# Performance work log

Measured on AMD Instinct MI355X. Metric: run time of the kernel, lower is better.

## Reference

```python
import jax, jax.numpy as jnp
import numpy as np

N = 50000
D = 128           # feature_dim
H = 8             # num_heads
DH = D // H       # head_dim = 16
K = 32            # k_neighbors
FFN = int(D * 1.5)  # 192
TAU_NEG = 0.6
BETA = 1.5
LN_EPS = 1e-5


def layer_norm(x, g, b):
    mu = jnp.mean(x, axis=-1, keepdims=True)
    var = jnp.mean((x - mu) ** 2, axis=-1, keepdims=True)
    return (x - mu) * jax.lax.rsqrt(var + LN_EPS) * g + b


def setup_inputs() -> dict:
    key = jax.random.key(0)
    ks = jax.random.split(key, 12)
    s = 1.0 / np.sqrt(D)
    inp = {
        "features": jax.random.normal(ks[0], (N, D), dtype=jnp.float32),
        "knn_indices": jax.random.randint(ks[1], (N, K), 0, N, dtype=jnp.int64 if jax.config.jax_enable_x64 else jnp.int32),
        "spatial_distances": jax.random.uniform(ks[2], (N, K), dtype=jnp.float32) * 8.0,
        "Wq": jax.random.normal(ks[3], (D, D), dtype=jnp.float32) * s,
        "Wk": jax.random.normal(ks[4], (D, D), dtype=jnp.float32) * s,
        "Wv": jax.random.normal(ks[5], (D, D), dtype=jnp.float32) * s,
        "Wo": jax.random.normal(ks[6], (D, D), dtype=jnp.float32) * s,
        "bo": jnp.zeros((D,), dtype=jnp.float32),
        "ln1_g": jnp.ones((D,), dtype=jnp.float32),
        "ln1_b": jnp.zeros((D,), dtype=jnp.float32),
        "W1": jax.random.normal(ks[7], (D, FFN), dtype=jnp.float32) * s,
        "b1": jnp.zeros((FFN,), dtype=jnp.float32),
        "W2": jax.random.normal(ks[8], (FFN, D), dtype=jnp.float32) * (1.0 / np.sqrt(FFN)),
        "b2": jnp.zeros((D,), dtype=jnp.float32),
        "ln2_g": jnp.ones((D,), dtype=jnp.float32),
        "ln2_b": jnp.zeros((D,), dtype=jnp.float32),
    }
    return inp


def reference(features, knn_indices, spatial_distances, Wq, Wk, Wv, Wo, bo,
              ln1_g, ln1_b, W1, b1, W2, b2, ln2_g, ln2_b):
    n = features.shape[0]
    Q = (features @ Wq).reshape(n, H, DH)           # (N,H,dh)
    Kp = (features @ Wk).reshape(n, H, DH)
    Vp = (features @ Wv).reshape(n, H, DH)

    K_local = Kp[knn_indices]                        # (N,K,H,dh) irregular gather
    V_local = Vp[knn_indices]                        # (N,K,H,dh)

    raw_scores = jnp.einsum("nhd,nkhd->nhk", Q, K_local) / np.sqrt(DH)  # (N,H,K)

    # per-head spatial decay: 1 / 2^(h+1)
    head_scalings = (0.5 ** jnp.arange(1, H + 1, dtype=features.dtype))  # (H,)
    scaled_dist = spatial_distances[:, None, :] * head_scalings[None, :, None]  # (N,H,K)

    attn_pos = jax.nn.softmax(raw_scores - scaled_dist, axis=-1)
    attn_neg = jax.nn.softmax((-raw_scores - scaled_dist) / TAU_NEG, axis=-1)
    attn = attn_pos - BETA * attn_neg                # (N,H,K); dropout is identity in eval

    attended = jnp.einsum("nhk,nkhd->nhd", attn, V_local).reshape(n, D)

    x = attended @ Wo + bo + features
    x = layer_norm(x, ln1_g, ln1_b)

    h = jax.nn.gelu(x @ W1 + b1, approximate=False)
    ffn_out = h @ W2 + b2
    out = layer_norm(ffn_out + x, ln2_g, ln2_b)
    return out
```

## Files before the change

### kernel.cpp

```cpp
#include <hip/hip_runtime.h>
#include <hip/hip_fp16.h>
#include <cmath>

typedef __attribute__((ext_vector_type(8))) _Float16 f16x8;
typedef __attribute__((ext_vector_type(4))) float f32x4;
typedef __attribute__((ext_vector_type(4))) unsigned int u32x4;

__device__ __forceinline__ unsigned int pkh(float a, float b) {
    __half2 h = __floats2half2_rn(a, b);
    return *(unsigned int*)&h;
}
__device__ __forceinline__ float gelu_fast(float x) {
    float w = x * fmaf(x * x, 0.1029377202f, 2.302085565f);
    return x * __builtin_amdgcn_rcpf(1.0f + exp2f(-w));
}
__device__ __forceinline__ __half2 shfl8h(__half2 x, int m) {
    int xi = *(int*)&x;
    int yi = __shfl_xor(xi, m, 8);
    return *(__half2*)&yi;
}

__global__ __launch_bounds__(256, 1) void k_prep(
    const float* __restrict__ Wq, const float* __restrict__ Wk, const float* __restrict__ Wv,
    const float* __restrict__ Wo, const float* __restrict__ W1, const float* __restrict__ W2,
    unsigned short* __restrict__ wsz)
{
    int idx = blockIdx.x * 256 + threadIdx.x;
    if (idx >= 28672) return;
    int f = idx >> 1;
    const int half = idx & 1;
    const float* W; unsigned short* dst; int M, KS, fl;
    if (f < 2048)       { W = Wq; dst = wsz;         M = 128; KS = 4; fl = f; }
    else if (f < 4096)  { W = Wk; dst = wsz + 16384; M = 128; KS = 4; fl = f - 2048; }
    else if (f < 6144)  { W = Wv; dst = wsz + 32768; M = 128; KS = 4; fl = f - 4096; }
    else if (f < 8192)  { W = Wo; dst = wsz + 49152; M = 128; KS = 4; fl = f - 6144; }
    else if (f < 11264) { W = W1; dst = wsz + 65536; M = 192; KS = 4; fl = f - 8192; }
    else                { W = W2; dst = wsz + 90112; M = 128; KS = 6; fl = f - 11264; }
    const int l  = fl & 63;
    const int ks = (fl >> 6) % KS;
    const int ct = (fl >> 6) / KS;
    const int k0 = ks * 32 + (l >> 4) * 8 + half * 4;
    const int col = ct * 16 + (l & 15);
    unsigned short tmp[4];
    #pragma unroll
    for (int j = 0; j < 4; ++j) {
        __half hh = __float2half(W[(size_t)(k0 + j) * M + col]);
        tmp[j] = *(unsigned short*)&hh;
    }
    ((uint2*)dst)[fl * 2 + half] = *(uint2*)tmp;
}

__global__ __launch_bounds__(256, 8) void k_qkv(
    const float* __restrict__ feat, const unsigned short* __restrict__ wsz,
    unsigned short* __restrict__ Qb, unsigned short* __restrict__ KVb, int n)
{
    const int w = threadIdx.x >> 6, lane = threadIdx.x & 63;
    const int lrow = lane & 15, kgrp = lane >> 4;
    const int node = blockIdx.x * 64 + w * 16 + lrow;
    const bool valid = node < n;

    f16x8 bfr[4];
    #pragma unroll
    for (int ks = 0; ks < 4; ++ks) {
        float4 lo = make_float4(0.f, 0.f, 0.f, 0.f), hi = lo;
        if (valid) {
            const float* p = feat + (size_t)node * 128 + ks * 32 + kgrp * 8;
            lo = *(const float4*)p;
            hi = *(const float4*)(p + 4);
        }
        f16x8 b;
        b[0] = (_Float16)lo.x; b[1] = (_Float16)lo.y; b[2] = (_Float16)lo.z; b[3] = (_Float16)lo.w;
        b[4] = (_Float16)hi.x; b[5] = (_Float16)hi.y; b[6] = (_Float16)hi.z; b[7] = (_Float16)hi.w;
        bfr[ks] = b;
    }

    for (int mat = 0; mat < 3; ++mat) {
        const unsigned short* wb = wsz + mat * 16384;
        f32x4 acc[8];
        #pragma unroll
        for (int ct = 0; ct < 8; ++ct) acc[ct] = (f32x4){0.f, 0.f, 0.f, 0.f};
        #pragma unroll
        for (int ct = 0; ct < 8; ++ct)
            #pragma unroll
            for (int ks = 0; ks < 4; ++ks) {
                f16x8 afr = *(const f16x8*)(wb + ((size_t)(ct * 4 + ks) * 64 + lane) * 8);
                acc[ct] = __builtin_amdgcn_mfma_f32_16x16x32_f16(afr, bfr[ks], acc[ct], 0, 0, 0);
            }
        if (valid) {
            unsigned short* O = (mat == 0) ? (Qb + (size_t)node * 128)
                              : (KVb + (size_t)node * 256 + (mat == 2 ? 128 : 0));
            #pragma unroll
            for (int ct = 0; ct < 8; ++ct) {
                int col = ct * 16 + kgrp * 4;
                *((uint2*)(O + col)) =
                    make_uint2(pkh(acc[ct][0], acc[ct][1]), pkh(acc[ct][2], acc[ct][3]));
            }
        }
    }
}

__global__ __launch_bounds__(256, 4) void k_attn(
    const unsigned short* __restrict__ Qb, const unsigned short* __restrict__ KVb,
    const int* __restrict__ knn, const float* __restrict__ dist,
    unsigned short* __restrict__ attf, int n)
{
    const int lane = threadIdx.x & 63;
    const int node = blockIdx.x * 4 + (threadIdx.x >> 6);
    if (node >= n) return;
    const int h = lane >> 3, r = lane & 7;
    const float L2E = 1.4426950408889634f;
    const float hsl = exp2f(-(float)(h + 1)) * L2E;

    int idx[4]; float sdl[4];
    #pragma unroll
    for (int jj = 0; jj < 4; ++jj) {
        int j = r + jj * 8;
        idx[jj] = __builtin_nontemporal_load(knn + (size_t)node * 32 + j);
        sdl[jj] = __builtin_nontemporal_load(dist + (size_t)node * 32 + j) * hsl;
    }

    const unsigned short* qp = Qb + (size_t)node * 128 + h * 16;
    __half2 q2[8];
    *((u32x4*)&q2[0]) = __builtin_nontemporal_load((const u32x4*)qp);
    *((u32x4*)&q2[4]) = __builtin_nontemporal_load((const u32x4*)(qp + 8));

    uint4 k0[4], k1[4], v0[4], v1[4];
    #pragma unroll
    for (int jj = 0; jj < 4; ++jj) {
        const unsigned short* kvp = KVb + (size_t)idx[jj] * 256 + h * 16;
        k0[jj] = *(const uint4*)kvp;
        k1[jj] = *(const uint4*)(kvp + 8);
        v0[jj] = *(const uint4*)(kvp + 128);
        v1[jj] = *(const uint4*)(kvp + 136);
    }

    float ap[4], an[4];
    #pragma unroll
    for (int jj = 0; jj < 4; ++jj) {
        const __half2* ka = (const __half2*)&k0[jj];
        const __half2* kb = (const __half2*)&k1[jj];
        __half2 s0 = __hmul2(q2[0], ka[0]);
        s0 = __hfma2(q2[1], ka[1], s0);
        s0 = __hfma2(q2[2], ka[2], s0);
        s0 = __hfma2(q2[3], ka[3], s0);
        __half2 s1 = __hmul2(q2[4], kb[0]);
        s1 = __hfma2(q2[5], kb[1], s1);
        s1 = __hfma2(q2[6], kb[2], s1);
        s1 = __hfma2(q2[7], kb[3], s1);
        float s = __low2float(s0) + __high2float(s0) + __low2float(s1) + __high2float(s1);
        float rawl = s * (0.25f * L2E);
        ap[jj] = rawl - sdl[jj];
        an[jj] = (-rawl - sdl[jj]) * (1.0f / 0.6f);
    }

    float mp = fmaxf(fmaxf(ap[0], ap[1]), fmaxf(ap[2], ap[3]));
    float mn = fmaxf(fmaxf(an[0], an[1]), fmaxf(an[2], an[3]));
    #pragma unroll
    for (int msk = 1; msk < 8; msk <<= 1) {
        mp = fmaxf(mp, __shfl_xor(mp, msk, 8));
        mn = fmaxf(mn, __shfl_xor(mn, msk, 8));
    }
    float ep[4], en[4], sp = 0.f, sn = 0.f;
    #pragma unroll
    for (int jj = 0; jj < 4; ++jj) {
        ep[jj] = exp2f(ap[jj] - mp); sp += ep[jj];
        en[jj] = exp2f(an[jj] - mn); sn += en[jj];
    }
    #pragma unroll
    for (int msk = 1; msk < 8; msk <<= 1) {
        sp += __shfl_xor(sp, msk, 8);
        sn += __shfl_xor(sn, msk, 8);
    }
    const float isp = 1.0f / sp;
    const float isn = 1.5f / sn;

    __half2 acc2[8];
    #pragma unroll
    for (int i = 0; i < 8; ++i) acc2[i] = __float2half2_rn(0.f);
    #pragma unroll
    for (int jj = 0; jj < 4; ++jj) {
        float wgt = ep[jj] * isp - en[jj] * isn;
        __half2 w2 = __float2half2_rn(wgt);
        const __half2* va = (const __half2*)&v0[jj];
        const __half2* vb = (const __half2*)&v1[jj];
        acc2[0] = __hfma2(w2, va[0], acc2[0]);
        acc2[1] = __hfma2(w2, va[1], acc2[1]);
        acc2[2] = __hfma2(w2, va[2], acc2[2]);
        acc2[3] = __hfma2(w2, va[3], acc2[3]);
        acc2[4] = __hfma2(w2, vb[0], acc2[4]);
        acc2[5] = __hfma2(w2, vb[1], acc2[5]);
        acc2[6] = __hfma2(w2, vb[2], acc2[6]);
        acc2[7] = __hfma2(w2, vb[3], acc2[7]);
    }
    #pragma unroll
    for (int i = 0; i < 8; ++i) {
        acc2[i] = __hadd2(acc2[i], shfl8h(acc2[i], 1));
        acc2[i] = __hadd2(acc2[i], shfl8h(acc2[i], 2));
        acc2[i] = __hadd2(acc2[i], shfl8h(acc2[i], 4));
    }
    if (r == 0) {
        const int g = node >> 4, lrow = node & 15;
        unsigned short* op = attf + (size_t)g * 2048 + (h >> 1) * 512 + (h & 1) * 256 + lrow * 8;
        __builtin_nontemporal_store(*(u32x4*)&acc2[0], (u32x4*)op);
        __builtin_nontemporal_store(*(u32x4*)&acc2[4], (u32x4*)(op + 128));
    }
}

__global__ __launch_bounds__(256, 4) void k_tail(
    const unsigned short* __restrict__ attf, const float* __restrict__ feat,
    const unsigned short* __restrict__ wsz,
    const float* __restrict__ bo, const float* __restrict__ g1, const float* __restrict__ b1ln,
    const float* __restrict__ b1f, const float* __restrict__ b2f,
    const float* __restrict__ g2, const float* __restrict__ b2ln,
    float* __restrict__ out, int n)
{
    __shared__ __align__(16) unsigned short hls[12288];
    const int tid = threadIdx.x;
    const int w = tid >> 6, lane = tid & 63;
    const int lrow = lane & 15, kgrp = lane >> 4;
    const int node = blockIdx.x * 64 + w * 16 + lrow;
    const bool valid = node < n;
    const int g = blockIdx.x * 4 + w;

    f16x8 bfr[6];
    #pragma unroll
    for (int ks = 0; ks < 4; ++ks) {
        uint4 u = make_uint4(0u, 0u, 0u, 0u);
        if (valid) u = *(const uint4*)(attf + (size_t)g * 2048 + (ks * 4 + kgrp) * 128 + lrow * 8);
        bfr[ks] = *(f16x8*)&u;
    }
    float4 fr[8];
    #pragma unroll
    for (int ct = 0; ct < 8; ++ct) {
        fr[ct] = make_float4(0.f, 0.f, 0.f, 0.f);
        if (valid) fr[ct] = *((const float4*)(feat + (size_t)node * 128 + ct * 16 + kgrp * 4));
    }

    const unsigned short* wo = wsz + 49152;
    f32x4 X[8];
    #pragma unroll
    for (int ct = 0; ct < 8; ++ct) {
        X[ct] = (f32x4){0.f, 0.f, 0.f, 0.f};
        #pragma unroll
        for (int ks = 0; ks < 4; ++ks) {
            f16x8 afr = *(const f16x8*)(wo + ((size_t)(ct * 4 + ks) * 64 + lane) * 8);
            X[ct] = __builtin_amdgcn_mfma_f32_16x16x32_f16(afr, bfr[ks], X[ct], 0, 0, 0);
        }
    }
    #pragma unroll
    for (int ct = 0; ct < 8; ++ct) {
        int col = ct * 16 + kgrp * 4;
        float4 bv = *((const float4*)(bo + col));
        X[ct][0] += bv.x + fr[ct].x; X[ct][1] += bv.y + fr[ct].y;
        X[ct][2] += bv.z + fr[ct].z; X[ct][3] += bv.w + fr[ct].w;
    }
    float s = 0.f;
    #pragma unroll
    for (int ct = 0; ct < 8; ++ct) s += X[ct][0] + X[ct][1] + X[ct][2] + X[ct][3];
    s += __shfl_xor(s, 16); s += __shfl_xor(s, 32);
    const float mu1 = s * (1.0f / 128.0f);
    float s2 = 0.f;
    #pragma unroll
    for (int ct = 0; ct < 8; ++ct)
        #pragma unroll
        for (int rr = 0; rr < 4; ++rr) { float d = X[ct][rr] - mu1; s2 = fmaf(d, d, s2); }
    s2 += __shfl_xor(s2, 16); s2 += __shfl_xor(s2, 32);
    const float rs1 = rsqrtf(s2 * (1.0f / 128.0f) + 1e-5f);

    uint2 xnh[8];
    #pragma unroll
    for (int ct = 0; ct < 8; ++ct) {
        int col = ct * 16 + kgrp * 4;
        float4 gg = *((const float4*)(g1 + col));
        float4 bb = *((const float4*)(b1ln + col));
        float x0 = (X[ct][0] - mu1) * rs1 * gg.x + bb.x;
        float x1 = (X[ct][1] - mu1) * rs1 * gg.y + bb.y;
        float x2 = (X[ct][2] - mu1) * rs1 * gg.z + bb.z;
        float x3 = (X[ct][3] - mu1) * rs1 * gg.w + bb.w;
        xnh[ct] = make_uint2(pkh(x0, x1), pkh(x2, x3));
        int ks4 = col >> 5, kg = (col & 31) >> 3, jb = col & 7;
        *((uint2*)&hls[w * 2048 + (ks4 * 4 + kg) * 128 + lrow * 8 + jb]) = xnh[ct];
    }
    __syncthreads();
    #pragma unroll
    for (int ks = 0; ks < 4; ++ks)
        bfr[ks] = *(const f16x8*)&hls[w * 2048 + (ks * 4 + kgrp) * 128 + lrow * 8];
    __syncthreads();

    const unsigned short* w1 = wsz + 65536;
    #pragma unroll
    for (int ct = 0; ct < 12; ++ct) {
        f32x4 acc = (f32x4){0.f, 0.f, 0.f, 0.f};
        #pragma unroll
        for (int ks = 0; ks < 4; ++ks) {
            f16x8 afr = *(const f16x8*)(w1 + ((size_t)(ct * 4 + ks) * 64 + lane) * 8);
            acc = __builtin_amdgcn_mfma_f32_16x16x32_f16(afr, bfr[ks], acc, 0, 0, 0);
        }
        int col = ct * 16 + kgrp * 4;
        float4 bv = *((const float4*)(b1f + col));
        float h0 = gelu_fast(acc[0] + bv.x), h1 = gelu_fast(acc[1] + bv.y);
        float h2 = gelu_fast(acc[2] + bv.z), h3 = gelu_fast(acc[3] + bv.w);
        int ks6 = col >> 5, kg = (col & 31) >> 3, jb = col & 7;
        *((uint2*)&hls[w * 3072 + (ks6 * 4 + kg) * 128 + lrow * 8 + jb]) =
            make_uint2(pkh(h0, h1), pkh(h2, h3));
    }
    __syncthreads();
    f16x8 bfh[6];
    #pragma unroll
    for (int ks = 0; ks < 6; ++ks)
        bfh[ks] = *(const f16x8*)&hls[w * 3072 + (ks * 4 + kgrp) * 128 + lrow * 8];

    const unsigned short* w2 = wsz + 90112;
    f32x4 Y[8];
    #pragma unroll
    for (int ct = 0; ct < 8; ++ct) {
        Y[ct] = (f32x4){0.f, 0.f, 0.f, 0.f};
        #pragma unroll
        for (int ks = 0; ks < 6; ++ks) {
            f16x8 afr = *(const f16x8*)(w2 + ((size_t)(ct * 6 + ks) * 64 + lane) * 8);
            Y[ct] = __builtin_amdgcn_mfma_f32_16x16x32_f16(afr, bfh[ks], Y[ct], 0, 0, 0);
        }
    }
    #pragma unroll
    for (int ct = 0; ct < 8; ++ct) {
        int col = ct * 16 + kgrp * 4;
        float4 bv = *((const float4*)(b2f + col));
        __half2 x01 = *(__half2*)&xnh[ct].x, x23 = *(__half2*)&xnh[ct].y;
        Y[ct][0] += bv.x + __low2float(x01);
        Y[ct][1] += bv.y + __high2float(x01);
        Y[ct][2] += bv.z + __low2float(x23);
        Y[ct][3] += bv.w + __high2float(x23);
    }
    float t1 = 0.f;
    #pragma unroll
    for (int ct = 0; ct < 8; ++ct) t1 += Y[ct][0] + Y[ct][1] + Y[ct][2] + Y[ct][3];
    t1 += __shfl_xor(t1, 16); t1 += __shfl_xor(t1, 32);
    const float mu2 = t1 * (1.0f / 128.0f);
    float t2 = 0.f;
    #pragma unroll
    for (int ct = 0; ct < 8; ++ct)
        #pragma unroll
        for (int rr = 0; rr < 4; ++rr) { float d = Y[ct][rr] - mu2; t2 = fmaf(d, d, t2); }
    t2 += __shfl_xor(t2, 16); t2 += __shfl_xor(t2, 32);
    const float rs2 = rsqrtf(t2 * (1.0f / 128.0f) + 1e-5f);
    if (valid) {
        #pragma unroll
        for (int ct = 0; ct < 8; ++ct) {
            int col = ct * 16 + kgrp * 4;
            float4 gg = *((const float4*)(g2 + col));
            float4 bb = *((const float4*)(b2ln + col));
            f32x4 o;
            o[0] = (Y[ct][0] - mu2) * rs2 * gg.x + bb.x;
            o[1] = (Y[ct][1] - mu2) * rs2 * gg.y + bb.y;
            o[2] = (Y[ct][2] - mu2) * rs2 * gg.z + bb.z;
            o[3] = (Y[ct][3] - mu2) * rs2 * gg.w + bb.w;
            __builtin_nontemporal_store(o, (f32x4*)(out + (size_t)node * 128 + col));
        }
    }
}

extern "C" void kernel_launch(void* const* d_in, const int* in_sizes, int n_in,
                              void* d_out, int out_size, void* d_ws, size_t ws_size,
                              hipStream_t stream)
{
    const float* feat = (const float*)d_in[0];
    const int*   knn  = (const int*)d_in[1];
    const float* dist = (const float*)d_in[2];
    const float* Wq   = (const float*)d_in[3];
    const float* Wk   = (const float*)d_in[4];
    const float* Wv   = (const float*)d_in[5];
    const float* Wo   = (const float*)d_in[6];
    const float* bo   = (const float*)d_in[7];
    const float* g1   = (const float*)d_in[8];
    const float* b1ln = (const float*)d_in[9];
    const float* W1   = (const float*)d_in[10];
    const float* b1f  = (const float*)d_in[11];
    const float* W2   = (const float*)d_in[12];
    const float* b2f  = (const float*)d_in[13];
    const float* g2   = (const float*)d_in[14];
    const float* b2ln = (const float*)d_in[15];
    float* out = (float*)d_out;

    const int n = in_sizes[0] / 128;
    const size_t ND = (size_t)n * 128;
    if (ws_size < 8 * ND + 262144) return;

    unsigned short* Qb   = (unsigned short*)d_ws;
    unsigned short* KVb  = Qb + ND;
    unsigned short* attf = KVb + 2 * ND;
    unsigned short* Wsz  = attf + ND;

    k_prep<<<112, 256, 0, stream>>>(Wq, Wk, Wv, Wo, W1, W2, Wsz);
    k_qkv <<<(n + 63) / 64, 256, 0, stream>>>(feat, Wsz, Qb, KVb, n);
    k_attn<<<(n + 3) / 4,   256, 0, stream>>>(Qb, KVb, knn, dist, attf, n);
    k_tail<<<(n + 63) / 64, 256, 0, stream>>>(attf, feat, Wsz, bo, g1, b1ln, b1f, b2f,
                                              g2, b2ln, out, n);
}
```

Before: 184.5 us.

## Make attention kernel grid-stride, drop nontemporal hints, retune launch bounds

The attention kernel becomes a grid-stride loop over a fixed grid of 2048 blocks with a launch-bounds occupancy hint of 6 instead of one block per four nodes. Nontemporal loads and stores are replaced by ordinary cached accesses in the attention and tail kernels. The QKV kernel's occupancy hint drops from 8 to 4, and the residual feature loads in the tail kernel move from an upfront register array into the bias-add loop. Together these aim to cut block launch overhead and register pressure and to let the caches keep data, at the risk of load imbalance or lost latency hiding.

```diff
diff --git a/kernel.cpp b/kernel.cpp
--- a/kernel.cpp
+++ b/kernel.cpp
@@ -4,7 +4,6 @@
 
 typedef __attribute__((ext_vector_type(8))) _Float16 f16x8;
 typedef __attribute__((ext_vector_type(4))) float f32x4;
-typedef __attribute__((ext_vector_type(4))) unsigned int u32x4;
 
 __device__ __forceinline__ unsigned int pkh(float a, float b) {
     __half2 h = __floats2half2_rn(a, b);
@@ -50,7 +49,7 @@
     ((uint2*)dst)[fl * 2 + half] = *(uint2*)tmp;
 }
 
-__global__ __launch_bounds__(256, 8) void k_qkv(
+__global__ __launch_bounds__(256, 4) void k_qkv(
     const float* __restrict__ feat, const unsigned short* __restrict__ wsz,
     unsigned short* __restrict__ Qb, unsigned short* __restrict__ KVb, int n)
 {
@@ -99,110 +98,111 @@
     }
 }
 
-__global__ __launch_bounds__(256, 4) void k_attn(
+__global__ __launch_bounds__(256, 6) void k_attn(
     const unsigned short* __restrict__ Qb, const unsigned short* __restrict__ KVb,
     const int* __restrict__ knn, const float* __restrict__ dist,
     unsigned short* __restrict__ attf, int n)
 {
     const int lane = threadIdx.x & 63;
-    const int node = blockIdx.x * 4 + (threadIdx.x >> 6);
-    if (node >= n) return;
     const int h = lane >> 3, r = lane & 7;
     const float L2E = 1.4426950408889634f;
     const float hsl = exp2f(-(float)(h + 1)) * L2E;
-
-    int idx[4]; float sdl[4];
-    #pragma unroll
-    for (int jj = 0; jj < 4; ++jj) {
-        int j = r + jj * 8;
-        idx[jj] = __builtin_nontemporal_load(knn + (size_t)node * 32 + j);
-        sdl[jj] = __builtin_nontemporal_load(dist + (size_t)node * 32 + j) * hsl;
-    }
-
-    const unsigned short* qp = Qb + (size_t)node * 128 + h * 16;
-    __half2 q2[8];
-    *((u32x4*)&q2[0]) = __builtin_nontemporal_load((const u32x4*)qp);
-    *((u32x4*)&q2[4]) = __builtin_nontemporal_load((const u32x4*)(qp + 8));
-
-    uint4 k0[4], k1[4], v0[4], v1[4];
-    #pragma unroll
-    for (int jj = 0; jj < 4; ++jj) {
-        const unsigned short* kvp = KVb + (size_t)idx[jj] * 256 + h * 16;
-        k0[jj] = *(const uint4*)kvp;
-        k1[jj] = *(const uint4*)(kvp + 8);
-        v0[jj] = *(const uint4*)(kvp + 128);
-        v1[jj] = *(const uint4*)(kvp + 136);
-    }
-
-    float ap[4], an[4];
-    #pragma unroll
-    for (int jj = 0; jj < 4; ++jj) {
-        const __half2* ka = (const __half2*)&k0[jj];
-        const __half2* kb = (const __half2*)&k1[jj];
-        __half2 s0 = __hmul2(q2[0], ka[0]);
-        s0 = __hfma2(q2[1], ka[1], s0);
-        s0 = __hfma2(q2[2], ka[2], s0);
-        s0 = __hfma2(q2[3], ka[3], s0);
-        __half2 s1 = __hmul2(q2[4], kb[0]);
-        s1 = __hfma2(q2[5], kb[1], s1);
-        s1 = __hfma2(q2[6], kb[2], s1);
-        s1 = __hfma2(q2[7], kb[3], s1);
-        float s = __low2float(s0) + __high2float(s0) + __low2float(s1) + __high2float(s1);
-        float rawl = s * (0.25f * L2E);
-        ap[jj] = rawl - sdl[jj];
-        an[jj] = (-rawl - sdl[jj]) * (1.0f / 0.6f);
-    }
-
-    float mp = fmaxf(fmaxf(ap[0], ap[1]), fmaxf(ap[2], ap[3]));
-    float mn = fmaxf(fmaxf(an[0], an[1]), fmaxf(an[2], an[3]));
-    #pragma unroll
-    for (int msk = 1; msk < 8; msk <<= 1) {
-        mp = fmaxf(mp, __shfl_xor(mp, msk, 8));
-        mn = fmaxf(mn, __shfl_xor(mn, msk, 8));
-    }
-    float ep[4], en[4], sp = 0.f, sn = 0.f;
-    #pragma unroll
-    for (int jj = 0; jj < 4; ++jj) {
-        ep[jj] = exp2f(ap[jj] - mp); sp += ep[jj];
-        en[jj] = exp2f(an[jj] - mn); sn += en[jj];
-    }
-    #pragma unroll
-    for (int msk = 1; msk < 8; msk <<= 1) {
-        sp += __shfl_xor(sp, msk, 8);
-        sn += __shfl_xor(sn, msk, 8);
-    }
-    const float isp = 1.0f / sp;
-    const float isn = 1.5f / sn;
-
-    __half2 acc2[8];
-    #pragma unroll
-    for (int i = 0; i < 8; ++i) acc2[i] = __float2half2_rn(0.f);
-    #pragma unroll
-    for (int jj = 0; jj < 4; ++jj) {
-        float wgt = ep[jj] * isp - en[jj] * isn;
-        __half2 w2 = __float2half2_rn(wgt);
-        const __half2* va = (const __half2*)&v0[jj];
-        const __half2* vb = (const __half2*)&v1[jj];
-        acc2[0] = __hfma2(w2, va[0], acc2[0]);
-        acc2[1] = __hfma2(w2, va[1], acc2[1]);
-        acc2[2] = __hfma2(w2, va[2], acc2[2]);
-        acc2[3] = __hfma2(w2, va[3], acc2[3]);
-        acc2[4] = __hfma2(w2, vb[0], acc2[4]);
-        acc2[5] = __hfma2(w2, vb[1], acc2[5]);
-        acc2[6] = __hfma2(w2, vb[2], acc2[6]);
-        acc2[7] = __hfma2(w2, vb[3], acc2[7]);
-    }
-    #pragma unroll
-    for (int i = 0; i < 8; ++i) {
-        acc2[i] = __hadd2(acc2[i], shfl8h(acc2[i], 1));
-        acc2[i] = __hadd2(acc2[i], shfl8h(acc2[i], 2));
-        acc2[i] = __hadd2(acc2[i], shfl8h(acc2[i], 4));
-    }
-    if (r == 0) {
-        const int g = node >> 4, lrow = node & 15;
-        unsigned short* op = attf + (size_t)g * 2048 + (h >> 1) * 512 + (h & 1) * 256 + lrow * 8;
-        __builtin_nontemporal_store(*(u32x4*)&acc2[0], (u32x4*)op);
-        __builtin_nontemporal_store(*(u32x4*)&acc2[4], (u32x4*)(op + 128));
+    const int stride = gridDim.x * 4;
+
+    for (int node = blockIdx.x * 4 + (threadIdx.x >> 6); node < n; node += stride) {
+        int idx[4]; float sdl[4];
+        #pragma unroll
+        for (int jj = 0; jj < 4; ++jj) {
+            int j = r + jj * 8;
+            idx[jj] = knn[(size_t)node * 32 + j];
+            sdl[jj] = dist[(size_t)node * 32 + j] * hsl;
+        }
+
+        const unsigned short* qp = Qb + (size_t)node * 128 + h * 16;
+        __half2 q2[8];
+        *((uint4*)&q2[0]) = *(const uint4*)qp;
+        *((uint4*)&q2[4]) = *(const uint4*)(qp + 8);
+
+        uint4 k0[4], k1[4], v0[4], v1[4];
+        #pragma unroll
+        for (int jj = 0; jj < 4; ++jj) {
+            const unsigned short* kvp = KVb + (size_t)idx[jj] * 256 + h * 16;
+            k0[jj] = *(const uint4*)kvp;
+            k1[jj] = *(const uint4*)(kvp + 8);
+            v0[jj] = *(const uint4*)(kvp + 128);
+            v1[jj] = *(const uint4*)(kvp + 136);
+        }
+
+        float ap[4], an[4];
+        #pragma unroll
+        for (int jj = 0; jj < 4; ++jj) {
+            const __half2* ka = (const __half2*)&k0[jj];
+            const __half2* kb = (const __half2*)&k1[jj];
+            __half2 s0 = __hmul2(q2[0], ka[0]);
+            s0 = __hfma2(q2[1], ka[1], s0);
+            s0 = __hfma2(q2[2], ka[2], s0);
+            s0 = __hfma2(q2[3], ka[3], s0);
+            __half2 s1 = __hmul2(q2[4], kb[0]);
+            s1 = __hfma2(q2[5], kb[1], s1);
+            s1 = __hfma2(q2[6], kb[2], s1);
+            s1 = __hfma2(q2[7], kb[3], s1);
+            float s = __low2float(s0) + __high2float(s0) + __low2float(s1) + __high2float(s1);
+            float rawl = s * (0.25f * L2E);
+            ap[jj] = rawl - sdl[jj];
+            an[jj] = (-rawl - sdl[jj]) * (1.0f / 0.6f);
+        }
+
+        float mp = fmaxf(fmaxf(ap[0], ap[1]), fmaxf(ap[2], ap[3]));
+        float mn = fmaxf(fmaxf(an[0], an[1]), fmaxf(an[2], an[3]));
+        #pragma unroll
+        for (int msk = 1; msk < 8; msk <<= 1) {
+            mp = fmaxf(mp, __shfl_xor(mp, msk, 8));
+            mn = fmaxf(mn, __shfl_xor(mn, msk, 8));
+        }
+        float ep[4], en[4], sp = 0.f, sn = 0.f;
+        #pragma unroll
+        for (int jj = 0; jj < 4; ++jj) {
+            ep[jj] = exp2f(ap[jj] - mp); sp += ep[jj];
+            en[jj] = exp2f(an[jj] - mn); sn += en[jj];
+        }
+        #pragma unroll
+        for (int msk = 1; msk < 8; msk <<= 1) {
+            sp += __shfl_xor(sp, msk, 8);
+            sn += __shfl_xor(sn, msk, 8);
+        }
+        const float isp = 1.0f / sp;
+        const float isn = 1.5f / sn;
+
+        __half2 acc2[8];
+        #pragma unroll
+        for (int i = 0; i < 8; ++i) acc2[i] = __float2half2_rn(0.f);
+        #pragma unroll
+        for (int jj = 0; jj < 4; ++jj) {
+            float wgt = ep[jj] * isp - en[jj] * isn;
+            __half2 w2 = __float2half2_rn(wgt);
+            const __half2* va = (const __half2*)&v0[jj];
+            const __half2* vb = (const __half2*)&v1[jj];
+            acc2[0] = __hfma2(w2, va[0], acc2[0]);
+            acc2[1] = __hfma2(w2, va[1], acc2[1]);
+            acc2[2] = __hfma2(w2, va[2], acc2[2]);
+            acc2[3] = __hfma2(w2, va[3], acc2[3]);
+            acc2[4] = __hfma2(w2, vb[0], acc2[4]);
+            acc2[5] = __hfma2(w2, vb[1], acc2[5]);
+            acc2[6] = __hfma2(w2, vb[2], acc2[6]);
+            acc2[7] = __hfma2(w2, vb[3], acc2[7]);
+        }
+        #pragma unroll
+        for (int i = 0; i < 8; ++i) {
+            acc2[i] = __hadd2(acc2[i], shfl8h(acc2[i], 1));
+            acc2[i] = __hadd2(acc2[i], shfl8h(acc2[i], 2));
+            acc2[i] = __hadd2(acc2[i], shfl8h(acc2[i], 4));
+        }
+        if (r == 0) {
+            const int g = node >> 4, lrow = node & 15;
+            unsigned short* op = attf + (size_t)g * 2048 + (h >> 1) * 512 + (h & 1) * 256 + lrow * 8;
+            *((uint4*)op)         = *(uint4*)&acc2[0];
+            *((uint4*)(op + 128)) = *(uint4*)&acc2[4];
+        }
     }
 }
 
@@ -229,13 +229,6 @@
         if (valid) u = *(const uint4*)(attf + (size_t)g * 2048 + (ks * 4 + kgrp) * 128 + lrow * 8);
         bfr[ks] = *(f16x8*)&u;
     }
-    float4 fr[8];
-    #pragma unroll
-    for (int ct = 0; ct < 8; ++ct) {
-        fr[ct] = make_float4(0.f, 0.f, 0.f, 0.f);
-        if (valid) fr[ct] = *((const float4*)(feat + (size_t)node * 128 + ct * 16 + kgrp * 4));
-    }
-
     const unsigned short* wo = wsz + 49152;
     f32x4 X[8];
     #pragma unroll
@@ -251,8 +244,10 @@
     for (int ct = 0; ct < 8; ++ct) {
         int col = ct * 16 + kgrp * 4;
         float4 bv = *((const float4*)(bo + col));
-        X[ct][0] += bv.x + fr[ct].x; X[ct][1] += bv.y + fr[ct].y;
-        X[ct][2] += bv.z + fr[ct].z; X[ct][3] += bv.w + fr[ct].w;
+        float4 fr = make_float4(0.f, 0.f, 0.f, 0.f);
+        if (valid) fr = *((const float4*)(feat + (size_t)node * 128 + col));
+        X[ct][0] += bv.x + fr.x; X[ct][1] += bv.y + fr.y;
+        X[ct][2] += bv.z + fr.z; X[ct][3] += bv.w + fr.w;
     }
     float s = 0.f;
     #pragma unroll
@@ -349,12 +344,12 @@
             int col = ct * 16 + kgrp * 4;
             float4 gg = *((const float4*)(g2 + col));
             float4 bb = *((const float4*)(b2ln + col));
-            f32x4 o;
-            o[0] = (Y[ct][0] - mu2) * rs2 * gg.x + bb.x;
-            o[1] = (Y[ct][1] - mu2) * rs2 * gg.y + bb.y;
-            o[2] = (Y[ct][2] - mu2) * rs2 * gg.z + bb.z;
-            o[3] = (Y[ct][3] - mu2) * rs2 * gg.w + bb.w;
-            __builtin_nontemporal_store(o, (f32x4*)(out + (size_t)node * 128 + col));
+            float4 o;
+            o.x = (Y[ct][0] - mu2) * rs2 * gg.x + bb.x;
+            o.y = (Y[ct][1] - mu2) * rs2 * gg.y + bb.y;
+            o.z = (Y[ct][2] - mu2) * rs2 * gg.z + bb.z;
+            o.w = (Y[ct][3] - mu2) * rs2 * gg.w + bb.w;
+            *((float4*)(out + (size_t)node * 128 + col)) = o;
         }
     }
 }
@@ -392,7 +387,7 @@
 
     k_prep<<<112, 256, 0, stream>>>(Wq, Wk, Wv, Wo, W1, W2, Wsz);
     k_qkv <<<(n + 63) / 64, 256, 0, stream>>>(feat, Wsz, Qb, KVb, n);
-    k_attn<<<(n + 3) / 4,   256, 0, stream>>>(Qb, KVb, knn, dist, attf, n);
+    k_attn<<<2048, 256, 0, stream>>>(Qb, KVb, knn, dist, attf, n);
     k_tail<<<(n + 63) / 64, 256, 0, stream>>>(attf, feat, Wsz, bo, g1, b1ln, b1f, b2f,
                                               g2, b2ln, out, n);
 }
```

New measurement: 195.7 us. 1.06x slower.
